# Kernel optimization log

Measured on AMD Instinct MI355X. Metric: run time of the kernel, lower is better.

## Reference

```python
import jax, jax.numpy as jnp
import numpy as np

B, T, D_Q, D_K, D_W = 128, 4096, 16, 16, 32


def setup_inputs() -> dict:
    key0 = jax.random.key(0)
    ks = jax.random.split(key0, 8)
    return {
        "query": jax.random.normal(ks[0], (B, 1, D_Q), dtype=jnp.float32),
        "key": jax.random.normal(ks[1], (B, T, D_K), dtype=jnp.float32),
        "value": jax.random.normal(ks[2], (B, T, D_K), dtype=jnp.float32),
        "W1": jax.random.normal(ks[3], (D_W, D_Q), dtype=jnp.float32) * 0.1,
        "W2": jax.random.normal(ks[4], (D_W, D_K), dtype=jnp.float32) * 0.1,
        "bias": jax.random.uniform(ks[5], (), dtype=jnp.float32, minval=-0.1, maxval=0.1),
        "v_w": jax.random.normal(ks[6], (1, D_W), dtype=jnp.float32) * 0.1,
        "v_b": jax.random.normal(ks[7], (1,), dtype=jnp.float32) * 0.1,
    }


def reference(query, key, value, W1, W2, bias, v_w, v_b):
    # Bahdanau additive attention.
    # query: [B,1,d_q], key/value: [B,T,d_k]
    q_proj = jnp.einsum('bqd,wd->bqw', query, W1)      # [B,1,d_w]
    k_proj = jnp.einsum('btd,wd->btw', key, W2)        # [B,T,d_w]
    h = jnp.tanh(k_proj + q_proj + bias)               # [B,T,d_w]
    score = (jnp.einsum('btw,ow->bto', h, v_w) + v_b).squeeze(-1)  # [B,T]
    attn = jax.nn.softmax(score, axis=-1)              # [B,T]
    context = jnp.einsum('bt,btd->bd', attn, value)[:, None, :]    # [B,1,d_v]
    return context, attn
```

## Files before the change

kernel.cpp:

```cpp
#include <hip/hip_runtime.h>

#define NB 128
#define NT 4096
#define DKD 16
#define DW 32
#define CHUNKS 4
#define TC 1024
#define BLK 256
#define PT 4

__device__ __forceinline__ float fast_tanh(float x) {
    float e = __expf(2.0f * x);
    return 1.0f - 2.0f * __builtin_amdgcn_rcpf(e + 1.0f);
}

__global__ __launch_bounds__(BLK) void aa_score(
    const float* __restrict__ query, const float* __restrict__ key,
    const float* __restrict__ value, const float* __restrict__ W1,
    const float* __restrict__ W2, const float* __restrict__ bias,
    const float* __restrict__ v_w, const float* __restrict__ v_b,
    float* __restrict__ attn,
    float* __restrict__ ws_l,
    float* __restrict__ ws_ctx)
{
    const int b   = blockIdx.x / CHUNKS;
    const int c   = blockIdx.x % CHUNKS;
    const int tid = threadIdx.x;

    __shared__ float s_w2[DW * DKD];
    __shared__ float s_comb[DW];
    __shared__ float s_vw[DW];
    __shared__ float s_rctx[4 * 16];
    __shared__ float s_rl[4];

    if (tid < 128)
        reinterpret_cast<float4*>(s_w2)[tid] = reinterpret_cast<const float4*>(W2)[tid];
    if (tid >= 128 && tid < 128 + DW) {
        const int w = tid - 128;
        float acc = bias[0];
        const float* q  = query + b * DKD;
        const float* w1 = W1 + w * DKD;
        #pragma unroll
        for (int d = 0; d < DKD; ++d) acc = fmaf(q[d], w1[d], acc);
        s_comb[w] = acc;
        s_vw[w]   = v_w[w];
    }
    __syncthreads();

    const float vb = v_b[0];
    const size_t tbase = (size_t)b * NT + (size_t)c * TC + (size_t)tid * PT;
    const float4* kp = reinterpret_cast<const float4*>(key)   + tbase * 4;
    const float4* vp = reinterpret_cast<const float4*>(value) + tbase * 4;

    float4 k0[PT], k1[PT], k2[PT], k3[PT];
    #pragma unroll
    for (int j = 0; j < PT; ++j) {
        k0[j] = kp[4*j + 0]; k1[j] = kp[4*j + 1];
        k2[j] = kp[4*j + 2]; k3[j] = kp[4*j + 3];
    }

    float sc[PT];
    #pragma unroll
    for (int j = 0; j < PT; ++j) sc[j] = vb;

    #pragma unroll 4
    for (int w = 0; w < DW; ++w) {
        const float4* wr = reinterpret_cast<const float4*>(s_w2 + w * DKD);
        const float4 w0 = wr[0], w1 = wr[1], w2 = wr[2], w3 = wr[3];
        const float cw = s_comb[w];
        const float vw = s_vw[w];
        #pragma unroll
        for (int j = 0; j < PT; ++j) {
            float h = cw;
            h = fmaf(k0[j].x, w0.x, h); h = fmaf(k0[j].y, w0.y, h);
            h = fmaf(k0[j].z, w0.z, h); h = fmaf(k0[j].w, w0.w, h);
            h = fmaf(k1[j].x, w1.x, h); h = fmaf(k1[j].y, w1.y, h);
            h = fmaf(k1[j].z, w1.z, h); h = fmaf(k1[j].w, w1.w, h);
            h = fmaf(k2[j].x, w2.x, h); h = fmaf(k2[j].y, w2.y, h);
            h = fmaf(k2[j].z, w2.z, h); h = fmaf(k2[j].w, w2.w, h);
            h = fmaf(k3[j].x, w3.x, h); h = fmaf(k3[j].y, w3.y, h);
            h = fmaf(k3[j].z, w3.z, h); h = fmaf(k3[j].w, w3.w, h);
            sc[j] = fmaf(fast_tanh(h), vw, sc[j]);
        }
    }

    float l = 0.0f;
    float ctx[16];
    #pragma unroll
    for (int d = 0; d < 16; ++d) ctx[d] = 0.0f;

    float p[PT];
    #pragma unroll
    for (int j = 0; j < PT; ++j) {
        p[j] = __expf(sc[j]);
        l += p[j];
        const float4 v0 = vp[4*j + 0], v1 = vp[4*j + 1];
        const float4 v2 = vp[4*j + 2], v3 = vp[4*j + 3];
        ctx[ 0] = fmaf(p[j], v0.x, ctx[ 0]); ctx[ 1] = fmaf(p[j], v0.y, ctx[ 1]);
        ctx[ 2] = fmaf(p[j], v0.z, ctx[ 2]); ctx[ 3] = fmaf(p[j], v0.w, ctx[ 3]);
        ctx[ 4] = fmaf(p[j], v1.x, ctx[ 4]); ctx[ 5] = fmaf(p[j], v1.y, ctx[ 5]);
        ctx[ 6] = fmaf(p[j], v1.z, ctx[ 6]); ctx[ 7] = fmaf(p[j], v1.w, ctx[ 7]);
        ctx[ 8] = fmaf(p[j], v2.x, ctx[ 8]); ctx[ 9] = fmaf(p[j], v2.y, ctx[ 9]);
        ctx[10] = fmaf(p[j], v2.z, ctx[10]); ctx[11] = fmaf(p[j], v2.w, ctx[11]);
        ctx[12] = fmaf(p[j], v3.x, ctx[12]); ctx[13] = fmaf(p[j], v3.y, ctx[13]);
        ctx[14] = fmaf(p[j], v3.z, ctx[14]); ctx[15] = fmaf(p[j], v3.w, ctx[15]);
    }
    reinterpret_cast<float4*>(attn + (size_t)b * NT + (size_t)c * TC)[tid] =
        make_float4(p[0], p[1], p[2], p[3]);

    #pragma unroll
    for (int o = 32; o > 0; o >>= 1) l += __shfl_xor(l, o);
    #pragma unroll
    for (int d = 0; d < 16; ++d) {
        #pragma unroll
        for (int o = 32; o > 0; o >>= 1) ctx[d] += __shfl_xor(ctx[d], o);
    }
    const int wave = tid >> 6;
    const int lane = tid & 63;
    if (lane == 0) {
        s_rl[wave] = l;
        #pragma unroll
        for (int d = 0; d < 16; ++d) s_rctx[wave * 16 + d] = ctx[d];
    }
    __syncthreads();
    const int slot = b * CHUNKS + c;
    if (tid < 16)
        ws_ctx[slot * 16 + tid] =
            s_rctx[tid] + s_rctx[16 + tid] + s_rctx[32 + tid] + s_rctx[48 + tid];
    if (tid == 0)
        ws_l[slot] = s_rl[0] + s_rl[1] + s_rl[2] + s_rl[3];
}

__global__ __launch_bounds__(BLK) void aa_finish(
    float* __restrict__ out,
    const float* __restrict__ ws_l,
    const float* __restrict__ ws_ctx)
{
    const int b   = blockIdx.x / CHUNKS;
    const int c   = blockIdx.x % CHUNKS;
    const int tid = threadIdx.x;
    const float L = ws_l[b*CHUNKS + 0] + ws_l[b*CHUNKS + 1] +
                    ws_l[b*CHUNKS + 2] + ws_l[b*CHUNKS + 3];
    const float inv = 1.0f / L;

    float4* ap = reinterpret_cast<float4*>(out + NB*DKD + (size_t)b * NT + (size_t)c * TC);
    float4 p = ap[tid];
    p.x *= inv; p.y *= inv; p.z *= inv; p.w *= inv;
    ap[tid] = p;

    if (c == 0 && tid < DKD) {
        const float* wc = ws_ctx + b * CHUNKS * 16;
        out[b * DKD + tid] = (wc[tid] + wc[16 + tid] + wc[32 + tid] + wc[48 + tid]) * inv;
    }
}

extern "C" void kernel_launch(void* const* d_in, const int* in_sizes, int n_in,
                              void* d_out, int out_size, void* d_ws, size_t ws_size,
                              hipStream_t stream) {
    const float* query = (const float*)d_in[0];
    const float* key   = (const float*)d_in[1];
    const float* value = (const float*)d_in[2];
    const float* W1    = (const float*)d_in[3];
    const float* W2    = (const float*)d_in[4];
    const float* bias  = (const float*)d_in[5];
    const float* v_w   = (const float*)d_in[6];
    const float* v_b   = (const float*)d_in[7];
    float* out = (float*)d_out;

    float* ws_l   = (float*)d_ws;
    float* ws_ctx = ws_l + NB * CHUNKS;

    aa_score<<<NB * CHUNKS, BLK, 0, stream>>>(
        query, key, value, W1, W2, bias, v_w, v_b,
        out + NB * DKD, ws_l, ws_ctx);
    aa_finish<<<NB * CHUNKS, BLK, 0, stream>>>(out, ws_l, ws_ctx);
}
```

Baseline: 116.5 us.

## Fuse score and normalize kernels via cooperative grid sync

Merges the score kernel and the normalization kernel into one cooperative launch. A grid-wide barrier sits between computing the per-chunk partial sums and normalizing. Unnormalized probabilities stay in registers, so the attn round trip through global memory (write, reread, rewrite) and the second launch go away. In exchange it relies on all 512 blocks being co-resident and pays for a grid barrier, which can cost more than a kernel boundary.

```diff
diff --git a/kernel.cpp b/kernel.cpp
--- a/kernel.cpp
+++ b/kernel.cpp
@@ -1,4 +1,7 @@
 #include <hip/hip_runtime.h>
+#include <hip/hip_cooperative_groups.h>
+
+namespace cg = cooperative_groups;
 
 #define NB 128
 #define NT 4096
@@ -14,12 +17,12 @@
     return 1.0f - 2.0f * __builtin_amdgcn_rcpf(e + 1.0f);
 }
 
-__global__ __launch_bounds__(BLK) void aa_score(
+__global__ __launch_bounds__(BLK) void aa_fused(
     const float* __restrict__ query, const float* __restrict__ key,
     const float* __restrict__ value, const float* __restrict__ W1,
     const float* __restrict__ W2, const float* __restrict__ bias,
     const float* __restrict__ v_w, const float* __restrict__ v_b,
-    float* __restrict__ attn,
+    float* __restrict__ out,
     float* __restrict__ ws_l,
     float* __restrict__ ws_ctx)
 {
@@ -105,8 +108,6 @@
         ctx[12] = fmaf(p[j], v3.x, ctx[12]); ctx[13] = fmaf(p[j], v3.y, ctx[13]);
         ctx[14] = fmaf(p[j], v3.z, ctx[14]); ctx[15] = fmaf(p[j], v3.w, ctx[15]);
     }
-    reinterpret_cast<float4*>(attn + (size_t)b * NT + (size_t)c * TC)[tid] =
-        make_float4(p[0], p[1], p[2], p[3]);
 
     #pragma unroll
     for (int o = 32; o > 0; o >>= 1) l += __shfl_xor(l, o);
@@ -129,24 +130,15 @@
             s_rctx[tid] + s_rctx[16 + tid] + s_rctx[32 + tid] + s_rctx[48 + tid];
     if (tid == 0)
         ws_l[slot] = s_rl[0] + s_rl[1] + s_rl[2] + s_rl[3];
-}
 
-__global__ __launch_bounds__(BLK) void aa_finish(
-    float* __restrict__ out,
-    const float* __restrict__ ws_l,
-    const float* __restrict__ ws_ctx)
-{
-    const int b   = blockIdx.x / CHUNKS;
-    const int c   = blockIdx.x % CHUNKS;
-    const int tid = threadIdx.x;
+    cg::this_grid().sync();
+
     const float L = ws_l[b*CHUNKS + 0] + ws_l[b*CHUNKS + 1] +
                     ws_l[b*CHUNKS + 2] + ws_l[b*CHUNKS + 3];
     const float inv = 1.0f / L;
 
-    float4* ap = reinterpret_cast<float4*>(out + NB*DKD + (size_t)b * NT + (size_t)c * TC);
-    float4 p = ap[tid];
-    p.x *= inv; p.y *= inv; p.z *= inv; p.w *= inv;
-    ap[tid] = p;
+    reinterpret_cast<float4*>(out + NB*DKD + (size_t)b * NT + (size_t)c * TC)[tid] =
+        make_float4(p[0]*inv, p[1]*inv, p[2]*inv, p[3]*inv);
 
     if (c == 0 && tid < DKD) {
         const float* wc = ws_ctx + b * CHUNKS * 16;
@@ -170,8 +162,11 @@
     float* ws_l   = (float*)d_ws;
     float* ws_ctx = ws_l + NB * CHUNKS;
 
-    aa_score<<<NB * CHUNKS, BLK, 0, stream>>>(
-        query, key, value, W1, W2, bias, v_w, v_b,
-        out + NB * DKD, ws_l, ws_ctx);
-    aa_finish<<<NB * CHUNKS, BLK, 0, stream>>>(out, ws_l, ws_ctx);
+    void* args[] = {
+        (void*)&query, (void*)&key, (void*)&value, (void*)&W1, (void*)&W2,
+        (void*)&bias, (void*)&v_w, (void*)&v_b, (void*)&out,
+        (void*)&ws_l, (void*)&ws_ctx,
+    };
+    hipLaunchCooperativeKernel(reinterpret_cast<void*>(aa_fused),
+                               dim3(NB * CHUNKS), dim3(BLK), args, 0, stream);
 }
```

After: 179.9 us. 1.54x slower.

## Split sequence into more chunks and prefetch value alongside key loads

Applied to the files above, without the earlier changes.

Doubles the number of chunks per batch row so each thread handles two timesteps instead of four, which gives 1024 blocks and raises memory-level parallelism. Value loads are issued up front with the key loads, before the barrier, so they overlap the tanh/score compute. W2 and v_w are read directly from global memory through uniform scalar loads instead of being staged in shared memory. The finish kernel is resized to match. The trade-off is more partial-sum traffic and register pressure from holding both key and value tiles at once.

```diff
diff --git a/kernel.cpp b/kernel.cpp
--- a/kernel.cpp
+++ b/kernel.cpp
@@ -4,17 +4,18 @@
 #define NT 4096
 #define DKD 16
 #define DW 32
-#define CHUNKS 4
-#define TC 1024
+#define CHUNKS 8
+#define TC 512
 #define BLK 256
-#define PT 4
+#define PT 2
+#define BLK2 128
 
 __device__ __forceinline__ float fast_tanh(float x) {
     float e = __expf(2.0f * x);
     return 1.0f - 2.0f * __builtin_amdgcn_rcpf(e + 1.0f);
 }
 
-__global__ __launch_bounds__(BLK) void aa_score(
+__global__ __launch_bounds__(BLK, 4) void aa_score(
     const float* __restrict__ query, const float* __restrict__ key,
     const float* __restrict__ value, const float* __restrict__ W1,
     const float* __restrict__ W2, const float* __restrict__ bias,
@@ -23,64 +24,64 @@
     float* __restrict__ ws_l,
     float* __restrict__ ws_ctx)
 {
-    const int b   = blockIdx.x / CHUNKS;
-    const int c   = blockIdx.x % CHUNKS;
+    const int b   = blockIdx.x >> 3;
+    const int c   = blockIdx.x & 7;
     const int tid = threadIdx.x;
 
-    __shared__ float s_w2[DW * DKD];
     __shared__ float s_comb[DW];
-    __shared__ float s_vw[DW];
     __shared__ float s_rctx[4 * 16];
     __shared__ float s_rl[4];
 
-    if (tid < 128)
-        reinterpret_cast<float4*>(s_w2)[tid] = reinterpret_cast<const float4*>(W2)[tid];
-    if (tid >= 128 && tid < 128 + DW) {
-        const int w = tid - 128;
+    if (tid < DW) {
+        const int w = tid;
         float acc = bias[0];
         const float* q  = query + b * DKD;
         const float* w1 = W1 + w * DKD;
         #pragma unroll
         for (int d = 0; d < DKD; ++d) acc = fmaf(q[d], w1[d], acc);
         s_comb[w] = acc;
-        s_vw[w]   = v_w[w];
     }
-    __syncthreads();
 
-    const float vb = v_b[0];
     const size_t tbase = (size_t)b * NT + (size_t)c * TC + (size_t)tid * PT;
     const float4* kp = reinterpret_cast<const float4*>(key)   + tbase * 4;
     const float4* vp = reinterpret_cast<const float4*>(value) + tbase * 4;
 
-    float4 k0[PT], k1[PT], k2[PT], k3[PT];
+    float4 ka[PT][4], va[PT][4];
     #pragma unroll
     for (int j = 0; j < PT; ++j) {
-        k0[j] = kp[4*j + 0]; k1[j] = kp[4*j + 1];
-        k2[j] = kp[4*j + 2]; k3[j] = kp[4*j + 3];
+        #pragma unroll
+        for (int r = 0; r < 4; ++r) ka[j][r] = kp[4*j + r];
+    }
+    #pragma unroll
+    for (int j = 0; j < PT; ++j) {
+        #pragma unroll
+        for (int r = 0; r < 4; ++r) va[j][r] = vp[4*j + r];
     }
 
+    __syncthreads();
+
+    const float vb = v_b[0];
     float sc[PT];
     #pragma unroll
     for (int j = 0; j < PT; ++j) sc[j] = vb;
 
-    #pragma unroll 4
+    #pragma unroll
     for (int w = 0; w < DW; ++w) {
-        const float4* wr = reinterpret_cast<const float4*>(s_w2 + w * DKD);
-        const float4 w0 = wr[0], w1 = wr[1], w2 = wr[2], w3 = wr[3];
-        const float cw = s_comb[w];
-        const float vw = s_vw[w];
+        const float* wr = W2 + w * DKD;
+        const float cw  = s_comb[w];
+        const float vww = v_w[w];
         #pragma unroll
         for (int j = 0; j < PT; ++j) {
             float h = cw;
-            h = fmaf(k0[j].x, w0.x, h); h = fmaf(k0[j].y, w0.y, h);
-            h = fmaf(k0[j].z, w0.z, h); h = fmaf(k0[j].w, w0.w, h);
-            h = fmaf(k1[j].x, w1.x, h); h = fmaf(k1[j].y, w1.y, h);
-            h = fmaf(k1[j].z, w1.z, h); h = fmaf(k1[j].w, w1.w, h);
-            h = fmaf(k2[j].x, w2.x, h); h = fmaf(k2[j].y, w2.y, h);
-            h = fmaf(k2[j].z, w2.z, h); h = fmaf(k2[j].w, w2.w, h);
-            h = fmaf(k3[j].x, w3.x, h); h = fmaf(k3[j].y, w3.y, h);
-            h = fmaf(k3[j].z, w3.z, h); h = fmaf(k3[j].w, w3.w, h);
-            sc[j] = fmaf(fast_tanh(h), vw, sc[j]);
+            h = fmaf(ka[j][0].x, wr[ 0], h); h = fmaf(ka[j][0].y, wr[ 1], h);
+            h = fmaf(ka[j][0].z, wr[ 2], h); h = fmaf(ka[j][0].w, wr[ 3], h);
+            h = fmaf(ka[j][1].x, wr[ 4], h); h = fmaf(ka[j][1].y, wr[ 5], h);
+            h = fmaf(ka[j][1].z, wr[ 6], h); h = fmaf(ka[j][1].w, wr[ 7], h);
+            h = fmaf(ka[j][2].x, wr[ 8], h); h = fmaf(ka[j][2].y, wr[ 9], h);
+            h = fmaf(ka[j][2].z, wr[10], h); h = fmaf(ka[j][2].w, wr[11], h);
+            h = fmaf(ka[j][3].x, wr[12], h); h = fmaf(ka[j][3].y, wr[13], h);
+            h = fmaf(ka[j][3].z, wr[14], h); h = fmaf(ka[j][3].w, wr[15], h);
+            sc[j] = fmaf(fast_tanh(h), vww, sc[j]);
         }
     }
 
@@ -94,19 +95,16 @@
     for (int j = 0; j < PT; ++j) {
         p[j] = __expf(sc[j]);
         l += p[j];
-        const float4 v0 = vp[4*j + 0], v1 = vp[4*j + 1];
-        const float4 v2 = vp[4*j + 2], v3 = vp[4*j + 3];
-        ctx[ 0] = fmaf(p[j], v0.x, ctx[ 0]); ctx[ 1] = fmaf(p[j], v0.y, ctx[ 1]);
-        ctx[ 2] = fmaf(p[j], v0.z, ctx[ 2]); ctx[ 3] = fmaf(p[j], v0.w, ctx[ 3]);
-        ctx[ 4] = fmaf(p[j], v1.x, ctx[ 4]); ctx[ 5] = fmaf(p[j], v1.y, ctx[ 5]);
-        ctx[ 6] = fmaf(p[j], v1.z, ctx[ 6]); ctx[ 7] = fmaf(p[j], v1.w, ctx[ 7]);
-        ctx[ 8] = fmaf(p[j], v2.x, ctx[ 8]); ctx[ 9] = fmaf(p[j], v2.y, ctx[ 9]);
-        ctx[10] = fmaf(p[j], v2.z, ctx[10]); ctx[11] = fmaf(p[j], v2.w, ctx[11]);
-        ctx[12] = fmaf(p[j], v3.x, ctx[12]); ctx[13] = fmaf(p[j], v3.y, ctx[13]);
-        ctx[14] = fmaf(p[j], v3.z, ctx[14]); ctx[15] = fmaf(p[j], v3.w, ctx[15]);
+        #pragma unroll
+        for (int r = 0; r < 4; ++r) {
+            ctx[4*r+0] = fmaf(p[j], va[j][r].x, ctx[4*r+0]);
+            ctx[4*r+1] = fmaf(p[j], va[j][r].y, ctx[4*r+1]);
+            ctx[4*r+2] = fmaf(p[j], va[j][r].z, ctx[4*r+2]);
+            ctx[4*r+3] = fmaf(p[j], va[j][r].w, ctx[4*r+3]);
+        }
     }
-    reinterpret_cast<float4*>(attn + (size_t)b * NT + (size_t)c * TC)[tid] =
-        make_float4(p[0], p[1], p[2], p[3]);
+    reinterpret_cast<float2*>(attn + (size_t)b * NT + (size_t)c * TC)[tid] =
+        make_float2(p[0], p[1]);
 
     #pragma unroll
     for (int o = 32; o > 0; o >>= 1) l += __shfl_xor(l, o);
@@ -131,16 +129,17 @@
         ws_l[slot] = s_rl[0] + s_rl[1] + s_rl[2] + s_rl[3];
 }
 
-__global__ __launch_bounds__(BLK) void aa_finish(
+__global__ __launch_bounds__(BLK2) void aa_finish(
     float* __restrict__ out,
     const float* __restrict__ ws_l,
     const float* __restrict__ ws_ctx)
 {
-    const int b   = blockIdx.x / CHUNKS;
-    const int c   = blockIdx.x % CHUNKS;
+    const int b   = blockIdx.x >> 3;
+    const int c   = blockIdx.x & 7;
     const int tid = threadIdx.x;
-    const float L = ws_l[b*CHUNKS + 0] + ws_l[b*CHUNKS + 1] +
-                    ws_l[b*CHUNKS + 2] + ws_l[b*CHUNKS + 3];
+    float L = 0.0f;
+    #pragma unroll
+    for (int i = 0; i < CHUNKS; ++i) L += ws_l[b * CHUNKS + i];
     const float inv = 1.0f / L;
 
     float4* ap = reinterpret_cast<float4*>(out + NB*DKD + (size_t)b * NT + (size_t)c * TC);
@@ -150,7 +149,10 @@
 
     if (c == 0 && tid < DKD) {
         const float* wc = ws_ctx + b * CHUNKS * 16;
-        out[b * DKD + tid] = (wc[tid] + wc[16 + tid] + wc[32 + tid] + wc[48 + tid]) * inv;
+        float s = 0.0f;
+        #pragma unroll
+        for (int i = 0; i < CHUNKS; ++i) s += wc[i * 16 + tid];
+        out[b * DKD + tid] = s * inv;
     }
 }
 
@@ -173,5 +175,5 @@
     aa_score<<<NB * CHUNKS, BLK, 0, stream>>>(
         query, key, value, W1, W2, bias, v_w, v_b,
         out + NB * DKD, ws_l, ws_ctx);
-    aa_finish<<<NB * CHUNKS, BLK, 0, stream>>>(out, ws_l, ws_ctx);
+    aa_finish<<<NB * CHUNKS, BLK2, 0, stream>>>(out, ws_l, ws_ctx);
 }
```

Result: slower. 119.3 us (+2.3%).
